# Performance work log

Measured on AMD Instinct MI355X. Metric: run time of the kernel, lower is better.

The kernel has to match this reference:

```python
import jax, jax.numpy as jnp
import numpy as np
import math

NUM_BUCKETS = 32
MAX_DISTANCE = 128
N_HEADS = 16
D_KV = 64


def _relative_position_bucket(relative_position, num_buckets=NUM_BUCKETS, max_distance=MAX_DISTANCE):
    # bidirectional (encoder) variant
    num_buckets //= 2
    relative_buckets = (relative_position > 0).astype(jnp.int32) * num_buckets
    rp = jnp.abs(relative_position)
    max_exact = num_buckets // 2
    is_small = rp < max_exact
    rp_large = max_exact + (
        jnp.log(jnp.maximum(rp, 1).astype(jnp.float32) / max_exact)
        / math.log(max_distance / max_exact)
        * (num_buckets - max_exact)
    ).astype(jnp.int32)
    rp_large = jnp.minimum(rp_large, num_buckets - 1)
    return relative_buckets + jnp.where(is_small, rp, rp_large)


def compute_bias(rel_bias, q_len, k_len):
    ctx = jnp.arange(q_len)[:, None]
    mem = jnp.arange(k_len)[None, :]
    buckets = _relative_position_bucket(mem - ctx)          # [q, k]
    values = rel_bias[buckets]                               # [q, k, h]
    return jnp.transpose(values, (2, 0, 1))[None]            # [1, h, q, k]


def setup_inputs() -> dict:
    key = jax.random.key(0)
    ks = jax.random.split(key, 6)
    d_model, inner = 1024, N_HEADS * D_KV
    s = 0.02
    return {
        "hidden_states": jax.random.normal(ks[0], (2, 2048, d_model), jnp.float32),
        "Wq": jax.random.normal(ks[1], (d_model, inner), jnp.float32) * s,
        "Wk": jax.random.normal(ks[2], (d_model, inner), jnp.float32) * s,
        "Wv": jax.random.normal(ks[3], (d_model, inner), jnp.float32) * s,
        "Wo": jax.random.normal(ks[4], (inner, d_model), jnp.float32) * s,
        "rel_bias": jax.random.normal(ks[5], (NUM_BUCKETS, N_HEADS), jnp.float32) * s,
    }


def reference(hidden_states, Wq, Wk, Wv, Wo, rel_bias):
    B, S, D = hidden_states.shape

    def split_heads(x):  # [B,S,inner] -> [B,H,S,dk]
        return x.reshape(B, S, N_HEADS, D_KV).transpose(0, 2, 1, 3)

    q = split_heads(hidden_states @ Wq)
    k = split_heads(hidden_states @ Wk)
    v = split_heads(hidden_states @ Wv)

    # T5 does NOT scale by 1/sqrt(d_kv)
    scores = jnp.einsum("bhqd,bhkd->bhqk", q, k)
    scores = scores + compute_bias(rel_bias, S, S)
    attn = jax.nn.softmax(scores, axis=-1)
    ctx = jnp.einsum("bhqk,bhkd->bhqd", attn, v)
    ctx = ctx.transpose(0, 2, 1, 3).reshape(B, S, N_HEADS * D_KV)
    return ctx @ Wo
```

## Files before the change

kernel.cpp:

```cpp
#include <hip/hip_runtime.h>
#include <hip/hip_bf16.h>

typedef __bf16 bf16x8 __attribute__((ext_vector_type(8)));
typedef __bf16 bf16x4 __attribute__((ext_vector_type(4)));
typedef float floatx4 __attribute__((ext_vector_type(4)));
using bf16 = __hip_bfloat16;

#define S_    2048
#define NHEAD 16
#define LOG2E 1.4426950408889634f

__device__ __forceinline__ void load_lds16(const bf16* g, void* lds) {
  __builtin_amdgcn_global_load_lds((const __attribute__((address_space(1))) void*)g,
                                   (__attribute__((address_space(3))) void*)lds, 16, 0, 0);
}

__global__ void cast_f32_bf16_kernel(const float* __restrict__ src, bf16* __restrict__ dst) {
  int i = (blockIdx.x * 256 + threadIdx.x) * 4;
  float4 v = *(const float4*)(src + i);
  bf16 o[4] = {__float2bfloat16(v.x), __float2bfloat16(v.y),
               __float2bfloat16(v.z), __float2bfloat16(v.w)};
  *(uint2*)(dst + i) = *(const uint2*)o;
}

__global__ void transpose_w_kernel(const float* __restrict__ wq, const float* __restrict__ wk,
                                   const float* __restrict__ wv, const float* __restrict__ wo,
                                   bf16* __restrict__ wt_qkv, bf16* __restrict__ wt_o) {
  __shared__ bf16 tile[32][33];
  int mat = blockIdx.z;
  const float* src = (mat == 0) ? wq : (mat == 1) ? wk : (mat == 2) ? wv : wo;
  bf16* dst = (mat == 3) ? wt_o : wt_qkv + mat * 1024 * 1024;
  int tx = threadIdx.x, ty = threadIdx.y;
  int n0 = blockIdx.x * 32, k0 = blockIdx.y * 32;
#pragma unroll
  for (int j = 0; j < 32; j += 8)
    tile[ty + j][tx] = __float2bfloat16(src[(k0 + ty + j) * 1024 + n0 + tx]);
  __syncthreads();
#pragma unroll
  for (int j = 0; j < 32; j += 8)
    dst[(n0 + ty + j) * 1024 + k0 + tx] = tile[tx][ty + j];
}

__global__ void bias_table_kernel(const float* __restrict__ rel_bias, float* __restrict__ tab) {
  int idx = blockIdx.x * 256 + threadIdx.x;
  int h = idx >> 12, j = idx & 4095;
  int delta = j - 2048;
  int rb = (delta > 0) ? 16 : 0;
  int rpa = delta < 0 ? -delta : delta;
  int bsmall;
  if (rpa < 8) {
    bsmall = rpa;
  } else {
    int lg = 25 - __clz(rpa * rpa);
    bsmall = 8 + lg;
    if (bsmall > 15) bsmall = 15;
  }
  tab[idx] = rel_bias[(rb + bsmall) * 16 + h] * LOG2E;
}

__global__ __launch_bounds__(256) void gemm_qkv_kernel(const bf16* __restrict__ A,
                                                       const bf16* __restrict__ Bt,
                                                       bf16* __restrict__ qh,
                                                       bf16* __restrict__ kh,
                                                       bf16* __restrict__ vh) {
  const int K = 1024;
  __shared__ bf16 As[128 * 32];
  __shared__ bf16 Bs[128 * 32];
  int t = threadIdx.x;
  int m0 = blockIdx.y * 128, n0 = blockIdx.x * 128;
  int w = t >> 6, lane = t & 63, ln = lane & 15, quad = lane >> 4;
  int wr = w >> 1, wc = w & 1;
  floatx4 acc[4][4];
  floatx4 zero = {0.f, 0.f, 0.f, 0.f};
#pragma unroll
  for (int i = 0; i < 4; i++)
#pragma unroll
    for (int j = 0; j < 4; j++) acc[i][j] = zero;

  int r = t >> 2, c = (t & 3) * 8;
  const bf16* Ag = A + (long)(m0 + r) * K + c;
  const bf16* Bg = Bt + (long)(n0 + r) * K + c;
  char* ldsA0 = (char*)As + w * 1024;
  char* ldsA1 = ldsA0 + 4096;
  char* ldsB0 = (char*)Bs + w * 1024;
  char* ldsB1 = ldsB0 + 4096;

  for (int k0 = 0; k0 < K; k0 += 32) {
    load_lds16(Ag + k0, ldsA0);
    load_lds16(Ag + (long)64 * K + k0, ldsA1);
    load_lds16(Bg + k0, ldsB0);
    load_lds16(Bg + (long)64 * K + k0, ldsB1);
    __syncthreads();
    bf16x8 af[4], bfv[4];
#pragma unroll
    for (int i = 0; i < 4; i++)
      af[i] = *(const bf16x8*)&As[(wr * 64 + i * 16 + ln) * 32 + quad * 8];
#pragma unroll
    for (int j = 0; j < 4; j++)
      bfv[j] = *(const bf16x8*)&Bs[(wc * 64 + j * 16 + ln) * 32 + quad * 8];
#pragma unroll
    for (int i = 0; i < 4; i++)
#pragma unroll
      for (int j = 0; j < 4; j++)
        acc[i][j] = __builtin_amdgcn_mfma_f32_16x16x32_bf16(af[i], bfv[j], acc[i][j], 0, 0, 0);
    __syncthreads();
  }

  int nb = n0 + wc * 64;
  int type = nb >> 10, h = (nb >> 6) & 15;
  bf16* dst = (type == 0) ? qh : (type == 1) ? kh : vh;
#pragma unroll
  for (int i = 0; i < 4; i++)
#pragma unroll
    for (int j = 0; j < 4; j++) {
      int d = j * 16 + ln;
#pragma unroll
      for (int rr = 0; rr < 4; rr++) {
        int sg = m0 + wr * 64 + i * 16 + quad * 4 + rr;
        int b = sg >> 11, s = sg & 2047;
        dst[((long)((b * 16 + h) * 2048 + s)) * 64 + d] = __float2bfloat16(acc[i][j][rr]);
      }
    }
}

__global__ void repack_kv_kernel(const bf16* __restrict__ kh, const bf16* __restrict__ vh,
                                 bf16* __restrict__ kf, bf16* __restrict__ vf) {
  __shared__ __bf16 vl[64 * 72];
  int bh = blockIdx.y, k0 = blockIdx.x * 64, t = threadIdx.x;
  long base = ((long)bh * 2048 + k0) * 64;

#pragma unroll
  for (int p = 0; p < 2; p++) {
    int c = t + p * 256;
    int blk16 = c >> 7, rem = c & 127;
    int f = rem >> 6, quad = (rem >> 4) & 3, ln = rem & 15;
    bf16x8 v = *(const bf16x8*)(kh + base + (blk16 * 16 + ln) * 64 + f * 32 + quad * 8);
    *(bf16x8*)(kf + base + blk16 * 1024 + f * 512 + quad * 128 + ln * 8) = v;
  }

#pragma unroll
  for (int p = 0; p < 2; p++) {
    int cc = t + p * 256;
    int row = cc >> 3, colc = cc & 7;
    *(bf16x8*)&vl[row * 72 + colc * 8] = *(const bf16x8*)(vh + base + row * 64 + colc * 8);
  }
  __syncthreads();
#pragma unroll
  for (int p = 0; p < 2; p++) {
    int c = t + p * 256;
    int blk32 = c >> 8, rem = c & 255;
    int dt = rem >> 6, quad = (rem >> 4) & 3, ln = rem & 15;
    int d = dt * 16 + ln;
    bf16x8 pk;
#pragma unroll
    for (int j = 0; j < 8; j++) pk[j] = vl[(blk32 * 32 + quad * 8 + j) * 72 + d];
    *(bf16x8*)(vf + base + blk32 * 2048 + dt * 512 + quad * 128 + ln * 8) = pk;
  }
}

__global__ __launch_bounds__(256, 2) void attn_kernel(const bf16* __restrict__ qh,
                                                      const bf16* __restrict__ kf,
                                                      const bf16* __restrict__ vf,
                                                      const float* __restrict__ btab,
                                                      bf16* __restrict__ ctx) {
  __shared__ char PsRaw[4 * 4096];
  int t = threadIdx.x, w = t >> 6, lane = t & 63, ln = lane & 15, quad = lane >> 4;
  int bh = blockIdx.y, b = bh >> 4, h = bh & 15;
  int qw = blockIdx.x * 128 + w * 32;

  const bf16* qbase = qh + (long)bh * S_ * 64;
  const bf16* kfb = kf + (long)bh * S_ * 64;
  const bf16* vfb = vf + (long)bh * S_ * 64;
  const float* bt = btab + h * 4096;
  char* myPs = PsRaw + w * 4096;
  int foff = quad * 128 + ln * 8;

  bf16x8 Qf[2][2];
#pragma unroll
  for (int g = 0; g < 2; g++) {
    const bf16* qr = qbase + (long)(qw + g * 16 + ln) * 64;
    Qf[g][0] = *(const bf16x8*)(qr + quad * 8);
    Qf[g][1] = *(const bf16x8*)(qr + 32 + quad * 8);
  }

  float cneg = bt[0], cpos = bt[4095];
  float l_acc[2] = {0.f, 0.f};
  floatx4 o[2][4];
  floatx4 zero = {0.f, 0.f, 0.f, 0.f};
#pragma unroll
  for (int g = 0; g < 2; g++)
#pragma unroll
    for (int dt = 0; dt < 4; dt++) o[g][dt] = zero;

  bf16x8 Kf_[4][2], Vc[4][2];
#pragma unroll
  for (int tile = 0; tile < 4; tile++) {
    Kf_[tile][0] = *(const bf16x8*)(kfb + tile * 1024 + foff);
    Kf_[tile][1] = *(const bf16x8*)(kfb + tile * 1024 + 512 + foff);
  }
#pragma unroll
  for (int f = 0; f < 2; f++)
#pragma unroll
    for (int dt = 0; dt < 4; dt++)
      Vc[dt][f] = *(const bf16x8*)(vfb + f * 2048 + dt * 512 + foff);

  for (int k0 = 0; k0 < S_; k0 += 64) {
    int kn = k0 + 64;
    bf16x8 Kn[4][2], Vn[4][2];
    if (kn < S_) {
      const bf16* kp = kfb + (long)kn * 64;
      const bf16* vp = vfb + (long)kn * 64;
#pragma unroll
      for (int tile = 0; tile < 4; tile++) {
        Kn[tile][0] = *(const bf16x8*)(kp + tile * 1024 + foff);
        Kn[tile][1] = *(const bf16x8*)(kp + tile * 1024 + 512 + foff);
      }
#pragma unroll
      for (int f = 0; f < 2; f++)
#pragma unroll
        for (int dt = 0; dt < 4; dt++)
          Vn[dt][f] = *(const bf16x8*)(vp + f * 2048 + dt * 512 + foff);
    }

    bool near = (k0 > qw - 192) && (k0 < qw + 192);
#pragma unroll
    for (int g = 0; g < 2; g++) {
      char* ps = myPs + g * 2048;
      floatx4 st[4];
#pragma unroll
      for (int tile = 0; tile < 4; tile++) {
        st[tile] = __builtin_amdgcn_mfma_f32_16x16x32_bf16(Kf_[tile][0], Qf[g][0], zero, 0, 0, 0);
        st[tile] = __builtin_amdgcn_mfma_f32_16x16x32_bf16(Kf_[tile][1], Qf[g][1], st[tile], 0, 0, 0);
      }
      if (near) {
#pragma unroll
        for (int tile = 0; tile < 4; tile++) {
          int bidx = k0 + tile * 16 + quad * 4 - (qw + g * 16 + ln) + 2048;
          float p0 = __builtin_amdgcn_exp2f(fmaf(st[tile][0], LOG2E, bt[bidx + 0]));
          float p1 = __builtin_amdgcn_exp2f(fmaf(st[tile][1], LOG2E, bt[bidx + 1]));
          float p2 = __builtin_amdgcn_exp2f(fmaf(st[tile][2], LOG2E, bt[bidx + 2]));
          float p3 = __builtin_amdgcn_exp2f(fmaf(st[tile][3], LOG2E, bt[bidx + 3]));
          l_acc[g] += (p0 + p1) + (p2 + p3);
          bf16x4 pk = {(__bf16)p0, (__bf16)p1, (__bf16)p2, (__bf16)p3};
          int chunk = tile * 2 + (quad >> 1);
          *(bf16x4*)(ps + (ln * 8 + (chunk ^ (ln & 7))) * 16 + (quad & 1) * 8) = pk;
        }
      } else {
        float cb = (k0 > qw) ? cpos : cneg;
#pragma unroll
        for (int tile = 0; tile < 4; tile++) {
          float p0 = __builtin_amdgcn_exp2f(fmaf(st[tile][0], LOG2E, cb));
          float p1 = __builtin_amdgcn_exp2f(fmaf(st[tile][1], LOG2E, cb));
          float p2 = __builtin_amdgcn_exp2f(fmaf(st[tile][2], LOG2E, cb));
          float p3 = __builtin_amdgcn_exp2f(fmaf(st[tile][3], LOG2E, cb));
          l_acc[g] += (p0 + p1) + (p2 + p3);
          bf16x4 pk = {(__bf16)p0, (__bf16)p1, (__bf16)p2, (__bf16)p3};
          int chunk = tile * 2 + (quad >> 1);
          *(bf16x4*)(ps + (ln * 8 + (chunk ^ (ln & 7))) * 16 + (quad & 1) * 8) = pk;
        }
      }
    }

#pragma unroll
    for (int g = 0; g < 2; g++) {
      char* ps = myPs + g * 2048;
      bf16x8 Pf0 = *(const bf16x8*)(ps + (ln * 8 + (quad ^ (ln & 7))) * 16);
      bf16x8 Pf1 = *(const bf16x8*)(ps + (ln * 8 + ((4 + quad) ^ (ln & 7))) * 16);
#pragma unroll
      for (int dt = 0; dt < 4; dt++) {
        o[g][dt] = __builtin_amdgcn_mfma_f32_16x16x32_bf16(Pf0, Vc[dt][0], o[g][dt], 0, 0, 0);
        o[g][dt] = __builtin_amdgcn_mfma_f32_16x16x32_bf16(Pf1, Vc[dt][1], o[g][dt], 0, 0, 0);
      }
    }

    if (kn < S_) {
#pragma unroll
      for (int tile = 0; tile < 4; tile++) {
        Kf_[tile][0] = Kn[tile][0]; Kf_[tile][1] = Kn[tile][1];
        Vc[tile][0] = Vn[tile][0];  Vc[tile][1] = Vn[tile][1];
      }
    }
  }

#pragma unroll
  for (int g = 0; g < 2; g++) {
    l_acc[g] += __shfl_xor(l_acc[g], 16);
    l_acc[g] += __shfl_xor(l_acc[g], 32);
  }
#pragma unroll
  for (int g = 0; g < 2; g++)
#pragma unroll
    for (int rr = 0; rr < 4; rr++) {
      float linv = 1.0f / __shfl(l_acc[g], quad * 4 + rr);
      int q = qw + g * 16 + quad * 4 + rr;
#pragma unroll
      for (int dt = 0; dt < 4; dt++)
        ctx[(long)(b * S_ + q) * 1024 + h * 64 + dt * 16 + ln] =
            __float2bfloat16(o[g][dt][rr] * linv);
    }
}

__global__ __launch_bounds__(256) void gemm_bt_kernel(const bf16* __restrict__ A,
                                                      const bf16* __restrict__ Bt,
                                                      float* __restrict__ C,
                                                      int M, int N, int K) {
  __shared__ bf16 As[128 * 32];
  __shared__ bf16 Bs[128 * 32];
  int t = threadIdx.x;
  int m0 = blockIdx.y * 128, n0 = blockIdx.x * 128;
  int w = t >> 6, lane = t & 63, ln = lane & 15, quad = lane >> 4;
  int wr = w >> 1, wc = w & 1;
  floatx4 acc[4][4];
  floatx4 zero = {0.f, 0.f, 0.f, 0.f};
#pragma unroll
  for (int i = 0; i < 4; i++)
#pragma unroll
    for (int j = 0; j < 4; j++) acc[i][j] = zero;

  int r = t >> 2, c = (t & 3) * 8;
  const bf16* Ag = A + (long)(m0 + r) * K + c;
  const bf16* Bg = Bt + (long)(n0 + r) * K + c;
  char* ldsA0 = (char*)As + w * 1024;
  char* ldsA1 = ldsA0 + 4096;
  char* ldsB0 = (char*)Bs + w * 1024;
  char* ldsB1 = ldsB0 + 4096;

  for (int k0 = 0; k0 < K; k0 += 32) {
    load_lds16(Ag + k0, ldsA0);
    load_lds16(Ag + (long)64 * K + k0, ldsA1);
    load_lds16(Bg + k0, ldsB0);
    load_lds16(Bg + (long)64 * K + k0, ldsB1);
    __syncthreads();
    bf16x8 af[4], bfv[4];
#pragma unroll
    for (int i = 0; i < 4; i++)
      af[i] = *(const bf16x8*)&As[(wr * 64 + i * 16 + ln) * 32 + quad * 8];
#pragma unroll
    for (int j = 0; j < 4; j++)
      bfv[j] = *(const bf16x8*)&Bs[(wc * 64 + j * 16 + ln) * 32 + quad * 8];
#pragma unroll
    for (int i = 0; i < 4; i++)
#pragma unroll
      for (int j = 0; j < 4; j++)
        acc[i][j] = __builtin_amdgcn_mfma_f32_16x16x32_bf16(af[i], bfv[j], acc[i][j], 0, 0, 0);
    __syncthreads();
  }

#pragma unroll
  for (int i = 0; i < 4; i++)
#pragma unroll
    for (int j = 0; j < 4; j++)
#pragma unroll
      for (int rr = 0; rr < 4; rr++)
        C[(long)(m0 + wr * 64 + i * 16 + quad * 4 + rr) * N + n0 + wc * 64 + j * 16 + ln] =
            acc[i][j][rr];
}

extern "C" void kernel_launch(void* const* d_in, const int* in_sizes, int n_in,
                              void* d_out, int out_size, void* d_ws, size_t ws_size,
                              hipStream_t stream) {
  (void)in_sizes; (void)n_in; (void)out_size; (void)ws_size;
  const float* hidden   = (const float*)d_in[0];
  const float* Wq       = (const float*)d_in[1];
  const float* Wk       = (const float*)d_in[2];
  const float* Wv       = (const float*)d_in[3];
  const float* Wo       = (const float*)d_in[4];
  const float* rel_bias = (const float*)d_in[5];

  char* ws = (char*)d_ws;
  bf16*  hbf    = (bf16*)(ws + 0);
  bf16*  wt_qkv = (bf16*)(ws + 8388608);
  bf16*  wt_o   = (bf16*)(ws + 14680064);
  float* btab   = (float*)(ws + 16777216);
  bf16*  qh     = (bf16*)(ws + 17039360);
  bf16*  kh     = (bf16*)(ws + 25427968);
  bf16*  vh     = (bf16*)(ws + 33816576);
  bf16*  kf     = (bf16*)(ws + 42205184);
  bf16*  vf     = (bf16*)(ws + 50593792);
  bf16*  ctx    = (bf16*)(ws + 58982400);

  cast_f32_bf16_kernel<<<dim3(4096), dim3(256), 0, stream>>>(hidden, hbf);
  transpose_w_kernel<<<dim3(32, 32, 4), dim3(32, 8), 0, stream>>>(Wq, Wk, Wv, Wo, wt_qkv, wt_o);
  bias_table_kernel<<<dim3(256), dim3(256), 0, stream>>>(rel_bias, btab);
  gemm_qkv_kernel<<<dim3(24, 32), dim3(256), 0, stream>>>(hbf, wt_qkv, qh, kh, vh);
  repack_kv_kernel<<<dim3(32, 32), dim3(256), 0, stream>>>(kh, vh, kf, vf);
  attn_kernel<<<dim3(16, 32), dim3(256), 0, stream>>>(qh, kf, vf, btab, ctx);
  gemm_bt_kernel<<<dim3(8, 32), dim3(256), 0, stream>>>(ctx, wt_o, (float*)d_out, 4096, 1024, 1024);
}
```

Measured before the change: 210.0 us.

## Stage shared K/V tiles in double-buffered LDS via direct global-to-LDS loads

The attention kernel now loads each 64-key K/V tile once per block into a double-buffered LDS area using global_load_lds. All four waves then read their MFMA fragments from LDS, where before each wave fetched the same K/V fragments from global memory into registers. The grid is also transposed so consecutive blocks share the same batch-head, which should help L2 reuse of K/V. In exchange, each iteration adds a block-wide barrier and LDS use grows by 32KB. Correctness depends on the async LDS loads having completed before that barrier.

```diff
diff --git a/kernel.cpp b/kernel.cpp
--- a/kernel.cpp
+++ b/kernel.cpp
@@ -164,16 +164,17 @@
                                                       const float* __restrict__ btab,
                                                       bf16* __restrict__ ctx) {
   __shared__ char PsRaw[4 * 4096];
+  __shared__ char KV[2][16384];
   int t = threadIdx.x, w = t >> 6, lane = t & 63, ln = lane & 15, quad = lane >> 4;
-  int bh = blockIdx.y, b = bh >> 4, h = bh & 15;
-  int qw = blockIdx.x * 128 + w * 32;
+  int bh = blockIdx.x, b = bh >> 4, h = bh & 15;
+  int qw = blockIdx.y * 128 + w * 32;
 
   const bf16* qbase = qh + (long)bh * S_ * 64;
   const bf16* kfb = kf + (long)bh * S_ * 64;
   const bf16* vfb = vf + (long)bh * S_ * 64;
   const float* bt = btab + h * 4096;
   char* myPs = PsRaw + w * 4096;
-  int foff = quad * 128 + ln * 8;
+  int lbo = quad * 256 + ln * 16;
 
   bf16x8 Qf[2][2];
 #pragma unroll
@@ -192,35 +193,42 @@
 #pragma unroll
     for (int dt = 0; dt < 4; dt++) o[g][dt] = zero;
 
-  bf16x8 Kf_[4][2], Vc[4][2];
-#pragma unroll
-  for (int tile = 0; tile < 4; tile++) {
-    Kf_[tile][0] = *(const bf16x8*)(kfb + tile * 1024 + foff);
-    Kf_[tile][1] = *(const bf16x8*)(kfb + tile * 1024 + 512 + foff);
-  }
-#pragma unroll
-  for (int f = 0; f < 2; f++)
-#pragma unroll
-    for (int dt = 0; dt < 4; dt++)
-      Vc[dt][f] = *(const bf16x8*)(vfb + f * 2048 + dt * 512 + foff);
-
+  {
+    const bf16* kg = kfb + t * 8;
+    const bf16* vg = vfb + t * 8;
+    load_lds16(kg,        KV[0] + w * 1024);
+    load_lds16(kg + 2048, KV[0] + 4096 + w * 1024);
+    load_lds16(vg,        KV[0] + 8192 + w * 1024);
+    load_lds16(vg + 2048, KV[0] + 12288 + w * 1024);
+  }
+
+  int pb = 0;
   for (int k0 = 0; k0 < S_; k0 += 64) {
+    __syncthreads();
     int kn = k0 + 64;
-    bf16x8 Kn[4][2], Vn[4][2];
     if (kn < S_) {
-      const bf16* kp = kfb + (long)kn * 64;
-      const bf16* vp = vfb + (long)kn * 64;
-#pragma unroll
-      for (int tile = 0; tile < 4; tile++) {
-        Kn[tile][0] = *(const bf16x8*)(kp + tile * 1024 + foff);
-        Kn[tile][1] = *(const bf16x8*)(kp + tile * 1024 + 512 + foff);
-      }
-#pragma unroll
-      for (int f = 0; f < 2; f++)
-#pragma unroll
-        for (int dt = 0; dt < 4; dt++)
-          Vn[dt][f] = *(const bf16x8*)(vp + f * 2048 + dt * 512 + foff);
-    }
+      const bf16* kg = kfb + (long)kn * 64 + t * 8;
+      const bf16* vg = vfb + (long)kn * 64 + t * 8;
+      char* nb_ = KV[pb ^ 1];
+      load_lds16(kg,        nb_ + w * 1024);
+      load_lds16(kg + 2048, nb_ + 4096 + w * 1024);
+      load_lds16(vg,        nb_ + 8192 + w * 1024);
+      load_lds16(vg + 2048, nb_ + 12288 + w * 1024);
+    }
+
+    const char* bK = KV[pb];
+    const char* bV = KV[pb] + 8192;
+    bf16x8 Kr[4][2], Vr[4][2];
+#pragma unroll
+    for (int tile = 0; tile < 4; tile++) {
+      Kr[tile][0] = *(const bf16x8*)(bK + tile * 2048 + lbo);
+      Kr[tile][1] = *(const bf16x8*)(bK + tile * 2048 + 1024 + lbo);
+    }
+#pragma unroll
+    for (int f = 0; f < 2; f++)
+#pragma unroll
+      for (int dt = 0; dt < 4; dt++)
+        Vr[dt][f] = *(const bf16x8*)(bV + f * 4096 + dt * 1024 + lbo);
 
     bool near = (k0 > qw - 192) && (k0 < qw + 192);
 #pragma unroll
@@ -229,8 +237,8 @@
       floatx4 st[4];
 #pragma unroll
       for (int tile = 0; tile < 4; tile++) {
-        st[tile] = __builtin_amdgcn_mfma_f32_16x16x32_bf16(Kf_[tile][0], Qf[g][0], zero, 0, 0, 0);
-        st[tile] = __builtin_amdgcn_mfma_f32_16x16x32_bf16(Kf_[tile][1], Qf[g][1], st[tile], 0, 0, 0);
+        st[tile] = __builtin_amdgcn_mfma_f32_16x16x32_bf16(Kr[tile][0], Qf[g][0], zero, 0, 0, 0);
+        st[tile] = __builtin_amdgcn_mfma_f32_16x16x32_bf16(Kr[tile][1], Qf[g][1], st[tile], 0, 0, 0);
       }
       if (near) {
 #pragma unroll
@@ -268,18 +276,12 @@
       bf16x8 Pf1 = *(const bf16x8*)(ps + (ln * 8 + ((4 + quad) ^ (ln & 7))) * 16);
 #pragma unroll
       for (int dt = 0; dt < 4; dt++) {
-        o[g][dt] = __builtin_amdgcn_mfma_f32_16x16x32_bf16(Pf0, Vc[dt][0], o[g][dt], 0, 0, 0);
-        o[g][dt] = __builtin_amdgcn_mfma_f32_16x16x32_bf16(Pf1, Vc[dt][1], o[g][dt], 0, 0, 0);
+        o[g][dt] = __builtin_amdgcn_mfma_f32_16x16x32_bf16(Pf0, Vr[dt][0], o[g][dt], 0, 0, 0);
+        o[g][dt] = __builtin_amdgcn_mfma_f32_16x16x32_bf16(Pf1, Vr[dt][1], o[g][dt], 0, 0, 0);
       }
     }
 
-    if (kn < S_) {
-#pragma unroll
-      for (int tile = 0; tile < 4; tile++) {
-        Kf_[tile][0] = Kn[tile][0]; Kf_[tile][1] = Kn[tile][1];
-        Vc[tile][0] = Vn[tile][0];  Vc[tile][1] = Vn[tile][1];
-      }
-    }
+    pb ^= 1;
   }
 
 #pragma unroll
@@ -384,6 +386,6 @@
   bias_table_kernel<<<dim3(256), dim3(256), 0, stream>>>(rel_bias, btab);
   gemm_qkv_kernel<<<dim3(24, 32), dim3(256), 0, stream>>>(hbf, wt_qkv, qh, kh, vh);
   repack_kv_kernel<<<dim3(32, 32), dim3(256), 0, stream>>>(kh, vh, kf, vf);
-  attn_kernel<<<dim3(16, 32), dim3(256), 0, stream>>>(qh, kf, vf, btab, ctx);
+  attn_kernel<<<dim3(32, 16), dim3(256), 0, stream>>>(qh, kf, vf, btab, ctx);
   gemm_bt_kernel<<<dim3(8, 32), dim3(256), 0, stream>>>(ctx, wt_o, (float*)d_out, 4096, 1024, 1024);
 }
```

After: 207.5 us. No clear change (-1.2%).

## Shrink attention per-wave query tile to 16 rows and double grid size

Applied to the files above, without the earlier changes.

Each wave now handles 16 query rows instead of 32, so the attention grid grows from 512 to 1024 blocks, launch bounds rise to 4 blocks per SM, and LDS per block is halved. The grid is also reordered so blockIdx.x walks heads and blockIdx.y walks query tiles. This cuts register pressure and raises occupancy and block count, which should improve latency hiding and load balance across CUs. The cost is that each K/V tile fetched into registers is reused by half as many queries, doubling K/V global traffic. The near-window bound is also tightened to match the smaller query span.

```diff
diff --git a/kernel.cpp b/kernel.cpp
--- a/kernel.cpp
+++ b/kernel.cpp
@@ -158,45 +158,42 @@
   }
 }
 
-__global__ __launch_bounds__(256, 2) void attn_kernel(const bf16* __restrict__ qh,
+__global__ __launch_bounds__(256, 4) void attn_kernel(const bf16* __restrict__ qh,
                                                       const bf16* __restrict__ kf,
                                                       const bf16* __restrict__ vf,
                                                       const float* __restrict__ btab,
                                                       bf16* __restrict__ ctx) {
-  __shared__ char PsRaw[4 * 4096];
+  __shared__ char PsRaw[4 * 2048];
   int t = threadIdx.x, w = t >> 6, lane = t & 63, ln = lane & 15, quad = lane >> 4;
-  int bh = blockIdx.y, b = bh >> 4, h = bh & 15;
-  int qw = blockIdx.x * 128 + w * 32;
+  int bh = blockIdx.x, b = bh >> 4, h = bh & 15;
+  int qw = blockIdx.y * 64 + w * 16;
 
   const bf16* qbase = qh + (long)bh * S_ * 64;
   const bf16* kfb = kf + (long)bh * S_ * 64;
   const bf16* vfb = vf + (long)bh * S_ * 64;
   const float* bt = btab + h * 4096;
-  char* myPs = PsRaw + w * 4096;
+  char* myPs = PsRaw + w * 2048;
   int foff = quad * 128 + ln * 8;
 
-  bf16x8 Qf[2][2];
-#pragma unroll
-  for (int g = 0; g < 2; g++) {
-    const bf16* qr = qbase + (long)(qw + g * 16 + ln) * 64;
-    Qf[g][0] = *(const bf16x8*)(qr + quad * 8);
-    Qf[g][1] = *(const bf16x8*)(qr + 32 + quad * 8);
+  bf16x8 Qf0, Qf1;
+  {
+    const bf16* qr = qbase + (long)(qw + ln) * 64;
+    Qf0 = *(const bf16x8*)(qr + quad * 8);
+    Qf1 = *(const bf16x8*)(qr + 32 + quad * 8);
   }
 
   float cneg = bt[0], cpos = bt[4095];
-  float l_acc[2] = {0.f, 0.f};
-  floatx4 o[2][4];
+  float l_acc = 0.f;
+  floatx4 o[4];
   floatx4 zero = {0.f, 0.f, 0.f, 0.f};
 #pragma unroll
-  for (int g = 0; g < 2; g++)
-#pragma unroll
-    for (int dt = 0; dt < 4; dt++) o[g][dt] = zero;
-
-  bf16x8 Kf_[4][2], Vc[4][2];
+  for (int dt = 0; dt < 4; dt++) o[dt] = zero;
+
+  bf16x8 Kc[4][2], Vc[4][2];
 #pragma unroll
   for (int tile = 0; tile < 4; tile++) {
-    Kf_[tile][0] = *(const bf16x8*)(kfb + tile * 1024 + foff);
-    Kf_[tile][1] = *(const bf16x8*)(kfb + tile * 1024 + 512 + foff);
+    Kc[tile][0] = *(const bf16x8*)(kfb + tile * 1024 + foff);
+    Kc[tile][1] = *(const bf16x8*)(kfb + tile * 1024 + 512 + foff);
   }
 #pragma unroll
   for (int f = 0; f < 2; f++)
@@ -222,82 +219,70 @@
           Vn[dt][f] = *(const bf16x8*)(vp + f * 2048 + dt * 512 + foff);
     }
 
-    bool near = (k0 > qw - 192) && (k0 < qw + 192);
-#pragma unroll
-    for (int g = 0; g < 2; g++) {
-      char* ps = myPs + g * 2048;
-      floatx4 st[4];
+    floatx4 st[4];
+#pragma unroll
+    for (int tile = 0; tile < 4; tile++) {
+      st[tile] = __builtin_amdgcn_mfma_f32_16x16x32_bf16(Kc[tile][0], Qf0, zero, 0, 0, 0);
+      st[tile] = __builtin_amdgcn_mfma_f32_16x16x32_bf16(Kc[tile][1], Qf1, st[tile], 0, 0, 0);
+    }
+
+    bool near = (k0 > qw - 192) && (k0 < qw + 144);
+    if (near) {
 #pragma unroll
       for (int tile = 0; tile < 4; tile++) {
-        st[tile] = __builtin_amdgcn_mfma_f32_16x16x32_bf16(Kf_[tile][0], Qf[g][0], zero, 0, 0, 0);
-        st[tile] = __builtin_amdgcn_mfma_f32_16x16x32_bf16(Kf_[tile][1], Qf[g][1], st[tile], 0, 0, 0);
-      }
-      if (near) {
-#pragma unroll
-        for (int tile = 0; tile < 4; tile++) {
-          int bidx = k0 + tile * 16 + quad * 4 - (qw + g * 16 + ln) + 2048;
-          float p0 = __builtin_amdgcn_exp2f(fmaf(st[tile][0], LOG2E, bt[bidx + 0]));
-          float p1 = __builtin_amdgcn_exp2f(fmaf(st[tile][1], LOG2E, bt[bidx + 1]));
-          float p2 = __builtin_amdgcn_exp2f(fmaf(st[tile][2], LOG2E, bt[bidx + 2]));
-          float p3 = __builtin_amdgcn_exp2f(fmaf(st[tile][3], LOG2E, bt[bidx + 3]));
-          l_acc[g] += (p0 + p1) + (p2 + p3);
-          bf16x4 pk = {(__bf16)p0, (__bf16)p1, (__bf16)p2, (__bf16)p3};
-          int chunk = tile * 2 + (quad >> 1);
-          *(bf16x4*)(ps + (ln * 8 + (chunk ^ (ln & 7))) * 16 + (quad & 1) * 8) = pk;
-        }
-      } else {
-        float cb = (k0 > qw) ? cpos : cneg;
-#pragma unroll
-        for (int tile = 0; tile < 4; tile++) {
-          float p0 = __builtin_amdgcn_exp2f(fmaf(st[tile][0], LOG2E, cb));
-          float p1 = __builtin_amdgcn_exp2f(fmaf(st[tile][1], LOG2E, cb));
-          float p2 = __builtin_amdgcn_exp2f(fmaf(st[tile][2], LOG2E, cb));
-          float p3 = __builtin_amdgcn_exp2f(fmaf(st[tile][3], LOG2E, cb));
-          l_acc[g] += (p0 + p1) + (p2 + p3);
-          bf16x4 pk = {(__bf16)p0, (__bf16)p1, (__bf16)p2, (__bf16)p3};
-          int chunk = tile * 2 + (quad >> 1);
-          *(bf16x4*)(ps + (ln * 8 + (chunk ^ (ln & 7))) * 16 + (quad & 1) * 8) = pk;
-        }
-      }
-    }
-
-#pragma unroll
-    for (int g = 0; g < 2; g++) {
-      char* ps = myPs + g * 2048;
-      bf16x8 Pf0 = *(const bf16x8*)(ps + (ln * 8 + (quad ^ (ln & 7))) * 16);
-      bf16x8 Pf1 = *(const bf16x8*)(ps + (ln * 8 + ((4 + quad) ^ (ln & 7))) * 16);
-#pragma unroll
-      for (int dt = 0; dt < 4; dt++) {
-        o[g][dt] = __builtin_amdgcn_mfma_f32_16x16x32_bf16(Pf0, Vc[dt][0], o[g][dt], 0, 0, 0);
-        o[g][dt] = __builtin_amdgcn_mfma_f32_16x16x32_bf16(Pf1, Vc[dt][1], o[g][dt], 0, 0, 0);
-      }
+        int bidx = k0 + tile * 16 + quad * 4 - (qw + ln) + 2048;
+        float p0 = __builtin_amdgcn_exp2f(fmaf(st[tile][0], LOG2E, bt[bidx + 0]));
+        float p1 = __builtin_amdgcn_exp2f(fmaf(st[tile][1], LOG2E, bt[bidx + 1]));
+        float p2 = __builtin_amdgcn_exp2f(fmaf(st[tile][2], LOG2E, bt[bidx + 2]));
+        float p3 = __builtin_amdgcn_exp2f(fmaf(st[tile][3], LOG2E, bt[bidx + 3]));
+        l_acc += (p0 + p1) + (p2 + p3);
+        bf16x4 pk = {(__bf16)p0, (__bf16)p1, (__bf16)p2, (__bf16)p3};
+        int chunk = tile * 2 + (quad >> 1);
+        *(bf16x4*)(myPs + (ln * 8 + (chunk ^ (ln & 7))) * 16 + (quad & 1) * 8) = pk;
+      }
+    } else {
+      float cb = (k0 > qw) ? cpos : cneg;
+#pragma unroll
+      for (int tile = 0; tile < 4; tile++) {
+        float p0 = __builtin_amdgcn_exp2f(fmaf(st[tile][0], LOG2E, cb));
+        float p1 = __builtin_amdgcn_exp2f(fmaf(st[tile][1], LOG2E, cb));
+        float p2 = __builtin_amdgcn_exp2f(fmaf(st[tile][2], LOG2E, cb));
+        float p3 = __builtin_amdgcn_exp2f(fmaf(st[tile][3], LOG2E, cb));
+        l_acc += (p0 + p1) + (p2 + p3);
+        bf16x4 pk = {(__bf16)p0, (__bf16)p1, (__bf16)p2, (__bf16)p3};
+        int chunk = tile * 2 + (quad >> 1);
+        *(bf16x4*)(myPs + (ln * 8 + (chunk ^ (ln & 7))) * 16 + (quad & 1) * 8) = pk;
+      }
+    }
+
+    bf16x8 Pf0 = *(const bf16x8*)(myPs + (ln * 8 + (quad ^ (ln & 7))) * 16);
+    bf16x8 Pf1 = *(const bf16x8*)(myPs + (ln * 8 + ((4 + quad) ^ (ln & 7))) * 16);
+#pragma unroll
+    for (int dt = 0; dt < 4; dt++) {
+      o[dt] = __builtin_amdgcn_mfma_f32_16x16x32_bf16(Pf0, Vc[dt][0], o[dt], 0, 0, 0);
+      o[dt] = __builtin_amdgcn_mfma_f32_16x16x32_bf16(Pf1, Vc[dt][1], o[dt], 0, 0, 0);
     }
 
     if (kn < S_) {
 #pragma unroll
       for (int tile = 0; tile < 4; tile++) {
-        Kf_[tile][0] = Kn[tile][0]; Kf_[tile][1] = Kn[tile][1];
-        Vc[tile][0] = Vn[tile][0];  Vc[tile][1] = Vn[tile][1];
-      }
-    }
-  }
-
-#pragma unroll
-  for (int g = 0; g < 2; g++) {
-    l_acc[g] += __shfl_xor(l_acc[g], 16);
-    l_acc[g] += __shfl_xor(l_acc[g], 32);
-  }
-#pragma unroll
-  for (int g = 0; g < 2; g++)
-#pragma unroll
-    for (int rr = 0; rr < 4; rr++) {
-      float linv = 1.0f / __shfl(l_acc[g], quad * 4 + rr);
-      int q = qw + g * 16 + quad * 4 + rr;
-#pragma unroll
-      for (int dt = 0; dt < 4; dt++)
-        ctx[(long)(b * S_ + q) * 1024 + h * 64 + dt * 16 + ln] =
-            __float2bfloat16(o[g][dt][rr] * linv);
-    }
+        Kc[tile][0] = Kn[tile][0]; Kc[tile][1] = Kn[tile][1];
+        Vc[tile][0] = Vn[tile][0]; Vc[tile][1] = Vn[tile][1];
+      }
+    }
+  }
+
+  l_acc += __shfl_xor(l_acc, 16);
+  l_acc += __shfl_xor(l_acc, 32);
+#pragma unroll
+  for (int rr = 0; rr < 4; rr++) {
+    float linv = 1.0f / __shfl(l_acc, quad * 4 + rr);
+    int q = qw + quad * 4 + rr;
+#pragma unroll
+    for (int dt = 0; dt < 4; dt++)
+      ctx[(long)(b * S_ + q) * 1024 + h * 64 + dt * 16 + ln] =
+          __float2bfloat16(o[dt][rr] * linv);
+  }
 }
 
 __global__ __launch_bounds__(256) void gemm_bt_kernel(const bf16* __restrict__ A,
@@ -384,6 +369,6 @@
   bias_table_kernel<<<dim3(256), dim3(256), 0, stream>>>(rel_bias, btab);
   gemm_qkv_kernel<<<dim3(24, 32), dim3(256), 0, stream>>>(hbf, wt_qkv, qh, kh, vh);
   repack_kv_kernel<<<dim3(32, 32), dim3(256), 0, stream>>>(kh, vh, kf, vf);
-  attn_kernel<<<dim3(16, 32), dim3(256), 0, stream>>>(qh, kf, vf, btab, ctx);
+  attn_kernel<<<dim3(32, 32), dim3(256), 0, stream>>>(qh, kf, vf, btab, ctx);
   gemm_bt_kernel<<<dim3(8, 32), dim3(256), 0, stream>>>(ctx, wt_o, (float*)d_out, 4096, 1024, 1024);
 }
```

After: 679.3 us. 3.23x slower.

## Fuse K/V repack into QKV GEMM epilogue and stage K through LDS

Applied to the files above, without the earlier changes.

The QKV GEMM epilogue now writes K and V straight into the MFMA-fragment layouts the attention kernel consumes, so the separate repack kernel and its extra global round trip go away. The attention kernel now double-buffers each K tile into shared memory with global_load_lds, shared by all four waves, instead of every wave loading K fragments from global memory into registers. It also swaps the grid dimensions so blocks of the same head run together, and tightens the near-diagonal window bound. The cost is a per-iteration __syncthreads and more shared memory, which may reduce occupancy.

```diff
diff --git a/kernel.cpp b/kernel.cpp
--- a/kernel.cpp
+++ b/kernel.cpp
@@ -61,8 +61,8 @@
 __global__ __launch_bounds__(256) void gemm_qkv_kernel(const bf16* __restrict__ A,
                                                        const bf16* __restrict__ Bt,
                                                        bf16* __restrict__ qh,
-                                                       bf16* __restrict__ kh,
-                                                       bf16* __restrict__ vh) {
+                                                       bf16* __restrict__ kf,
+                                                       bf16* __restrict__ vf) {
   const int K = 1024;
   __shared__ bf16 As[128 * 32];
   __shared__ bf16 Bs[128 * 32];
@@ -108,53 +108,45 @@
 
   int nb = n0 + wc * 64;
   int type = nb >> 10, h = (nb >> 6) & 15;
-  bf16* dst = (type == 0) ? qh : (type == 1) ? kh : vh;
-#pragma unroll
-  for (int i = 0; i < 4; i++)
-#pragma unroll
-    for (int j = 0; j < 4; j++) {
-      int d = j * 16 + ln;
-#pragma unroll
-      for (int rr = 0; rr < 4; rr++) {
-        int sg = m0 + wr * 64 + i * 16 + quad * 4 + rr;
-        int b = sg >> 11, s = sg & 2047;
-        dst[((long)((b * 16 + h) * 2048 + s)) * 64 + d] = __float2bfloat16(acc[i][j][rr]);
-      }
-    }
-}
-
-__global__ void repack_kv_kernel(const bf16* __restrict__ kh, const bf16* __restrict__ vh,
-                                 bf16* __restrict__ kf, bf16* __restrict__ vf) {
-  __shared__ __bf16 vl[64 * 72];
-  int bh = blockIdx.y, k0 = blockIdx.x * 64, t = threadIdx.x;
-  long base = ((long)bh * 2048 + k0) * 64;
-
-#pragma unroll
-  for (int p = 0; p < 2; p++) {
-    int c = t + p * 256;
-    int blk16 = c >> 7, rem = c & 127;
-    int f = rem >> 6, quad = (rem >> 4) & 3, ln = rem & 15;
-    bf16x8 v = *(const bf16x8*)(kh + base + (blk16 * 16 + ln) * 64 + f * 32 + quad * 8);
-    *(bf16x8*)(kf + base + blk16 * 1024 + f * 512 + quad * 128 + ln * 8) = v;
-  }
-
-#pragma unroll
-  for (int p = 0; p < 2; p++) {
-    int cc = t + p * 256;
-    int row = cc >> 3, colc = cc & 7;
-    *(bf16x8*)&vl[row * 72 + colc * 8] = *(const bf16x8*)(vh + base + row * 64 + colc * 8);
-  }
-  __syncthreads();
-#pragma unroll
-  for (int p = 0; p < 2; p++) {
-    int c = t + p * 256;
-    int blk32 = c >> 8, rem = c & 255;
-    int dt = rem >> 6, quad = (rem >> 4) & 3, ln = rem & 15;
-    int d = dt * 16 + ln;
-    bf16x8 pk;
-#pragma unroll
-    for (int j = 0; j < 8; j++) pk[j] = vl[(blk32 * 32 + quad * 8 + j) * 72 + d];
-    *(bf16x8*)(vf + base + blk32 * 2048 + dt * 512 + quad * 128 + ln * 8) = pk;
+  int b = (m0 >> 11);
+  int sl0 = (m0 & 2047) + wr * 64;
+  long bhbase = (long)((b * 16 + h)) * 131072;
+
+  if (type == 0) {
+#pragma unroll
+    for (int i = 0; i < 4; i++)
+#pragma unroll
+      for (int j = 0; j < 4; j++) {
+        int d = j * 16 + ln;
+#pragma unroll
+        for (int rr = 0; rr < 4; rr++) {
+          int s = sl0 + i * 16 + quad * 4 + rr;
+          qh[bhbase + (long)s * 64 + d] = __float2bfloat16(acc[i][j][rr]);
+        }
+      }
+  } else if (type == 1) {
+#pragma unroll
+    for (int i = 0; i < 4; i++)
+#pragma unroll
+      for (int j = 0; j < 4; j++) {
+        int d = j * 16 + ln;
+        int dpart = (d >> 5) * 512 + ((d >> 3) & 3) * 128 + (d & 7);
+        int kb = (sl0 + i * 16) * 64;
+#pragma unroll
+        for (int rr = 0; rr < 4; rr++)
+          kf[bhbase + kb + dpart + (quad * 4 + rr) * 8] = __float2bfloat16(acc[i][j][rr]);
+      }
+  } else {
+#pragma unroll
+    for (int i = 0; i < 4; i++)
+#pragma unroll
+      for (int j = 0; j < 4; j++) {
+        int off = (sl0 + (i >> 1) * 32) * 64 + j * 512 +
+                  ((quad >> 1) + ((i & 1) << 1)) * 128 + ln * 8 + (quad & 1) * 4;
+        bf16x4 pk = {(__bf16)acc[i][j][0], (__bf16)acc[i][j][1],
+                     (__bf16)acc[i][j][2], (__bf16)acc[i][j][3]};
+        *(bf16x4*)(vf + bhbase + off) = pk;
+      }
   }
 }
 
@@ -164,15 +156,17 @@
                                                       const float* __restrict__ btab,
                                                       bf16* __restrict__ ctx) {
   __shared__ char PsRaw[4 * 4096];
+  __shared__ char Ks[2][8192];
   int t = threadIdx.x, w = t >> 6, lane = t & 63, ln = lane & 15, quad = lane >> 4;
-  int bh = blockIdx.y, b = bh >> 4, h = bh & 15;
-  int qw = blockIdx.x * 128 + w * 32;
+  int bh = blockIdx.x, b = bh >> 4, h = bh & 15;
+  int qw = blockIdx.y * 128 + w * 32;
 
   const bf16* qbase = qh + (long)bh * S_ * 64;
   const bf16* kfb = kf + (long)bh * S_ * 64;
   const bf16* vfb = vf + (long)bh * S_ * 64;
   const float* bt = btab + h * 4096;
   char* myPs = PsRaw + w * 4096;
+  int lbo = quad * 256 + ln * 16;
   int foff = quad * 128 + ln * 8;
 
   bf16x8 Qf[2][2];
@@ -192,29 +186,24 @@
 #pragma unroll
     for (int dt = 0; dt < 4; dt++) o[g][dt] = zero;
 
-  bf16x8 Kf_[4][2], Vc[4][2];
-#pragma unroll
-  for (int tile = 0; tile < 4; tile++) {
-    Kf_[tile][0] = *(const bf16x8*)(kfb + tile * 1024 + foff);
-    Kf_[tile][1] = *(const bf16x8*)(kfb + tile * 1024 + 512 + foff);
-  }
+  load_lds16(kfb + t * 8, Ks[0] + w * 1024);
+  load_lds16(kfb + 2048 + t * 8, Ks[0] + 4096 + w * 1024);
+  bf16x8 Vc[4][2], Vn[4][2];
 #pragma unroll
   for (int f = 0; f < 2; f++)
 #pragma unroll
     for (int dt = 0; dt < 4; dt++)
       Vc[dt][f] = *(const bf16x8*)(vfb + f * 2048 + dt * 512 + foff);
 
+  int pb = 0;
   for (int k0 = 0; k0 < S_; k0 += 64) {
+    __syncthreads();
     int kn = k0 + 64;
-    bf16x8 Kn[4][2], Vn[4][2];
     if (kn < S_) {
-      const bf16* kp = kfb + (long)kn * 64;
+      const bf16* kg = kfb + (long)kn * 64 + t * 8;
+      load_lds16(kg, Ks[pb ^ 1] + w * 1024);
+      load_lds16(kg + 2048, Ks[pb ^ 1] + 4096 + w * 1024);
       const bf16* vp = vfb + (long)kn * 64;
-#pragma unroll
-      for (int tile = 0; tile < 4; tile++) {
-        Kn[tile][0] = *(const bf16x8*)(kp + tile * 1024 + foff);
-        Kn[tile][1] = *(const bf16x8*)(kp + tile * 1024 + 512 + foff);
-      }
 #pragma unroll
       for (int f = 0; f < 2; f++)
 #pragma unroll
@@ -222,15 +211,23 @@
           Vn[dt][f] = *(const bf16x8*)(vp + f * 2048 + dt * 512 + foff);
     }
 
-    bool near = (k0 > qw - 192) && (k0 < qw + 192);
+    const char* bK = Ks[pb];
+    bf16x8 Kr[4][2];
+#pragma unroll
+    for (int tile = 0; tile < 4; tile++) {
+      Kr[tile][0] = *(const bf16x8*)(bK + tile * 2048 + lbo);
+      Kr[tile][1] = *(const bf16x8*)(bK + tile * 2048 + 1024 + lbo);
+    }
+
+    bool near = (k0 > qw - 192) && (k0 < qw + 160);
 #pragma unroll
     for (int g = 0; g < 2; g++) {
       char* ps = myPs + g * 2048;
       floatx4 st[4];
 #pragma unroll
       for (int tile = 0; tile < 4; tile++) {
-        st[tile] = __builtin_amdgcn_mfma_f32_16x16x32_bf16(Kf_[tile][0], Qf[g][0], zero, 0, 0, 0);
-        st[tile] = __builtin_amdgcn_mfma_f32_16x16x32_bf16(Kf_[tile][1], Qf[g][1], st[tile], 0, 0, 0);
+        st[tile] = __builtin_amdgcn_mfma_f32_16x16x32_bf16(Kr[tile][0], Qf[g][0], zero, 0, 0, 0);
+        st[tile] = __builtin_amdgcn_mfma_f32_16x16x32_bf16(Kr[tile][1], Qf[g][1], st[tile], 0, 0, 0);
       }
       if (near) {
 #pragma unroll
@@ -275,11 +272,11 @@
 
     if (kn < S_) {
 #pragma unroll
-      for (int tile = 0; tile < 4; tile++) {
-        Kf_[tile][0] = Kn[tile][0]; Kf_[tile][1] = Kn[tile][1];
-        Vc[tile][0] = Vn[tile][0];  Vc[tile][1] = Vn[tile][1];
-      }
-    }
+      for (int dt = 0; dt < 4; dt++) {
+        Vc[dt][0] = Vn[dt][0]; Vc[dt][1] = Vn[dt][1];
+      }
+    }
+    pb ^= 1;
   }
 
 #pragma unroll
@@ -373,17 +370,14 @@
   bf16*  wt_o   = (bf16*)(ws + 14680064);
   float* btab   = (float*)(ws + 16777216);
   bf16*  qh     = (bf16*)(ws + 17039360);
-  bf16*  kh     = (bf16*)(ws + 25427968);
-  bf16*  vh     = (bf16*)(ws + 33816576);
-  bf16*  kf     = (bf16*)(ws + 42205184);
-  bf16*  vf     = (bf16*)(ws + 50593792);
-  bf16*  ctx    = (bf16*)(ws + 58982400);
+  bf16*  kf     = (bf16*)(ws + 25427968);
+  bf16*  vf     = (bf16*)(ws + 33816576);
+  bf16*  ctx    = (bf16*)(ws + 42205184);
 
   cast_f32_bf16_kernel<<<dim3(4096), dim3(256), 0, stream>>>(hidden, hbf);
   transpose_w_kernel<<<dim3(32, 32, 4), dim3(32, 8), 0, stream>>>(Wq, Wk, Wv, Wo, wt_qkv, wt_o);
   bias_table_kernel<<<dim3(256), dim3(256), 0, stream>>>(rel_bias, btab);
-  gemm_qkv_kernel<<<dim3(24, 32), dim3(256), 0, stream>>>(hbf, wt_qkv, qh, kh, vh);
-  repack_kv_kernel<<<dim3(32, 32), dim3(256), 0, stream>>>(kh, vh, kf, vf);
-  attn_kernel<<<dim3(16, 32), dim3(256), 0, stream>>>(qh, kf, vf, btab, ctx);
+  gemm_qkv_kernel<<<dim3(24, 32), dim3(256), 0, stream>>>(hbf, wt_qkv, qh, kf, vf);
+  attn_kernel<<<dim3(32, 16), dim3(256), 0, stream>>>(qh, kf, vf, btab, ctx);
   gemm_bt_kernel<<<dim3(8, 32), dim3(256), 0, stream>>>(ctx, wt_o, (float*)d_out, 4096, 1024, 1024);
 }
```

Result: no change. 206.6 us (-1.6%).
